# Performance work log

Measured on AMD Instinct MI355X. Metric: run time of the kernel, lower is better.

Reference implementation:

```python
import jax, jax.numpy as jnp
import numpy as np

N_QUBITS = 5
N_A = 1
N_LAYERS = 4
PATCH = 2 ** (N_QUBITS - N_A)  # 16

CNOT4 = jnp.array([[1, 0, 0, 0], [0, 1, 0, 0], [0, 0, 0, 1], [0, 0, 1, 0]], dtype=jnp.complex64)


def _ry(t):
    c = jnp.cos(t / 2).astype(jnp.complex64)
    s = jnp.sin(t / 2).astype(jnp.complex64)
    return jnp.stack([jnp.stack([c, -s]), jnp.stack([s, c])])


def _rot(phi, theta, omega):
    # PennyLane Rot = RZ(omega) RY(theta) RZ(phi)
    c = jnp.cos(theta / 2)
    s = jnp.sin(theta / 2)
    ep = jnp.exp(-0.5j * (phi + omega))  # e^{-i(phi+omega)/2}
    em = jnp.exp(-0.5j * (phi - omega))  # e^{-i(phi-omega)/2}
    return jnp.stack([jnp.stack([ep * c, -jnp.conj(em) * s]),
                      jnp.stack([em * s, jnp.conj(ep) * c])])


def _apply_1q(state, U, w):
    # contract U onto qubit axis w of state [2]*5
    s = jnp.tensordot(U, state, axes=(1, w))
    return jnp.moveaxis(s, 0, w)


def _apply_cnot(state, c, t):
    perm = jnp.moveaxis(state, (c, t), (0, 1))
    shp = perm.shape
    out = (CNOT4 @ perm.reshape(4, -1)).reshape(shp)
    return jnp.moveaxis(out, (0, 1), (c, t))


def _simulate(noise, w):
    # noise: [5], w: [4,5,3] -> normalized probs over first 16 basis states
    state = jnp.zeros((2,) * N_QUBITS, jnp.complex64).at[(0,) * N_QUBITS].set(1.0)
    for q in range(N_QUBITS):
        state = _apply_1q(state, _ry(noise[q]), q)
    for l in range(N_LAYERS):
        r = l % (N_QUBITS - 1) + 1  # StronglyEntanglingLayers default ranges
        for q in range(N_QUBITS):
            state = _apply_1q(state, _rot(w[l, q, 0], w[l, q, 1], w[l, q, 2]), q)
        for q in range(N_QUBITS):
            state = _apply_cnot(state, q, (q + r) % N_QUBITS)
    probs = jnp.abs(state.reshape(-1)) ** 2  # [32]
    p0 = probs[:PATCH] / jnp.sum(probs)  # partial measure: ancilla wire 4 == 0
    return p0 / jnp.max(p0)


def setup_inputs() -> dict:
    key = jax.random.key(0)
    k1, k2 = jax.random.split(key)
    B, G = 65536, 4
    x = jax.random.uniform(k1, (B, N_QUBITS), dtype=jnp.float32)
    weights = jax.random.uniform(k2, (G, N_LAYERS, N_QUBITS, 3), dtype=jnp.float32)  # q_delta=1
    return {"x": x, "weights": weights}


def reference(x, weights):
    sim_g = jax.vmap(_simulate, in_axes=(None, 0))   # over generators
    sim_bg = jax.vmap(sim_g, in_axes=(0, None))      # over batch
    out = sim_bg(x, weights)                         # [B, G, 16]
    return out.reshape(x.shape[0], -1).astype(jnp.float32)  # [B, G*16]
```

## Files before the change

kernel.cpp:

```cpp
#include <hip/hip_runtime.h>


#define NGEN 4
#define NLAY 4
#define NQ   5

typedef _Float16 half8 __attribute__((ext_vector_type(8)));
typedef float    f32x4 __attribute__((ext_vector_type(4)));

__global__ __launch_bounds__(256) void pqg_fused(
    const float* __restrict__ x,
    const float* __restrict__ wts,
    float* __restrict__ out)
{
    __shared__ float gm[NLAY * NQ * 8];
    __shared__ float Mr[16 * 33];
    __shared__ float Mi[16 * 33];
    __shared__ __align__(16) _Float16 afr[512];
    __shared__ __align__(16) _Float16 afi[512];
    __shared__ float scC[512 * 5];
    __shared__ float scS[512 * 5];

    const int t  = threadIdx.x;
    const int g  = blockIdx.x & 3;
    const int b0 = (blockIdx.x >> 2) * 512;

    {
        const float2* xb = (const float2*)(x + (size_t)b0 * 5);
#pragma unroll
        for (int i = 0; i < 5; ++i) {
            const int e = i * 256 + t;
            const float2 v = xb[e];
            scS[2 * e + 0] = __sinf(0.5f * v.x);
            scC[2 * e + 0] = __cosf(0.5f * v.x);
            scS[2 * e + 1] = __sinf(0.5f * v.y);
            scC[2 * e + 1] = __cosf(0.5f * v.y);
        }
    }

    if (t < NLAY * NQ) {
        const float* wp = wts + (g * (NLAY * NQ) + t) * 3;
        const float phi = wp[0], theta = wp[1], omega = wp[2];
        const float a = 0.5f * (phi + omega);
        const float bb = 0.5f * (phi - omega);
        const float h = 0.5f * theta;
        const float sa = __sinf(a), ca = __cosf(a);
        const float sb = __sinf(bb), cb = __cosf(bb);
        const float st = __sinf(h), ct = __cosf(h);
        float* m = &gm[t * 8];
        m[0] =  ca * ct;  m[1] = -sa * ct;
        m[2] = -cb * st;  m[3] = -sb * st;
        m[4] =  cb * st;  m[5] = -sb * st;
        m[6] =  ca * ct;  m[7] =  sa * ct;
    }

#pragma unroll
    for (int h = 0; h < 2; ++h) {
        const int idx = h * 256 + t;
        const int r = idx >> 5, c = idx & 31;
        Mr[r * 33 + c] = (r == c) ? 1.0f : 0.0f;
        Mi[r * 33 + c] = 0.0f;
    }
    __syncthreads();

    const int row = t & 15;
    const int p   = t >> 4;

#pragma clang loop unroll(disable)
    for (int l = NLAY - 1; l >= 0; --l) {
        {
            const int c0 = p, c1 = p + 16;
            int v0 = c0, v1 = c1;
#pragma unroll
            for (int q = 0; q < NQ; ++q) {
                const int cb = 16 >> q;
                int tq = q + l + 1; if (tq >= NQ) tq -= NQ;
                const int tb = 16 >> tq;
                if (v0 & cb) v0 ^= tb;
                if (v1 & cb) v1 ^= tb;
            }
            const float a0r = Mr[row * 33 + v0], a0i = Mi[row * 33 + v0];
            const float a1r = Mr[row * 33 + v1], a1i = Mi[row * 33 + v1];
            __syncthreads();
            Mr[row * 33 + c0] = a0r;  Mi[row * 33 + c0] = a0i;
            Mr[row * 33 + c1] = a1r;  Mi[row * 33 + c1] = a1i;
            __syncthreads();
        }
#pragma clang loop unroll(disable)
        for (int q = NQ - 1; q >= 0; --q) {
            const float* m = &gm[(l * NQ + q) * 8];
            const float u00r = m[0], u00i = m[1], u01r = m[2], u01i = m[3];
            const float u10r = m[4], u10i = m[5], u11r = m[6], u11i = m[7];
            const int sb = 16 >> q;
            const int lowm = sb - 1;
            const int i = ((p & ~lowm) << 1) | (p & lowm);
            const int j = i | sb;
            const int ii = row * 33 + i, jj = row * 33 + j;
            const float ar = Mr[ii], ai = Mi[ii];
            const float br = Mr[jj], bi = Mi[jj];
            Mr[ii] = u00r * ar - u00i * ai + u10r * br - u10i * bi;
            Mi[ii] = u00r * ai + u00i * ar + u10r * bi + u10i * br;
            Mr[jj] = u01r * ar - u01i * ai + u11r * br - u11i * bi;
            Mi[jj] = u01r * ai + u01i * ar + u11r * bi + u11i * br;
            __syncthreads();
        }
    }

#pragma unroll
    for (int h = 0; h < 2; ++h) {
        const int idx = h * 256 + t;
        const int k = idx >> 4, m = idx & 15;
        const int L = (k >> 3) * 16 + m;
        const int jj = k & 7;
        afr[L * 8 + jj] = (_Float16)Mr[m * 33 + k];
        afi[L * 8 + jj] = (_Float16)Mi[m * 33 + k];
    }
    __syncthreads();

    const int lane = t & 63;
    const int wv   = t >> 6;
    const int quad = lane >> 4;
    const int n    = lane & 15;

    const half8 Ar = *(const half8*)&afr[lane * 8];
    const half8 Ai = *(const half8*)&afi[lane * 8];

#pragma unroll
    for (int t8 = 0; t8 < 8; ++t8) {
        const int bl = wv * 128 + t8 * 16 + n;
        const int b  = b0 + bl;
        const float* C = &scC[bl * 5];
        const float* S = &scS[bl * 5];

        const float f01 = ((quad & 2) ? S[0] : C[0]) * ((quad & 1) ? S[1] : C[1]);
        const float a0 = f01 * C[2], a1 = f01 * S[2];
        const float b00 = a0 * C[3], b01 = a0 * S[3];
        const float b10 = a1 * C[3], b11 = a1 * S[3];

        half8 Bf;
        Bf[0] = (_Float16)(b00 * C[4]);  Bf[1] = (_Float16)(b00 * S[4]);
        Bf[2] = (_Float16)(b01 * C[4]);  Bf[3] = (_Float16)(b01 * S[4]);
        Bf[4] = (_Float16)(b10 * C[4]);  Bf[5] = (_Float16)(b10 * S[4]);
        Bf[6] = (_Float16)(b11 * C[4]);  Bf[7] = (_Float16)(b11 * S[4]);

        f32x4 accR = {0.f, 0.f, 0.f, 0.f};
        f32x4 accI = {0.f, 0.f, 0.f, 0.f};
        accR = __builtin_amdgcn_mfma_f32_16x16x32_f16(Ar, Bf, accR, 0, 0, 0);
        accI = __builtin_amdgcn_mfma_f32_16x16x32_f16(Ai, Bf, accI, 0, 0, 0);

        const float p0 = accR[0] * accR[0] + accI[0] * accI[0];
        const float p1 = accR[1] * accR[1] + accI[1] * accI[1];
        const float p2 = accR[2] * accR[2] + accI[2] * accI[2];
        const float p3 = accR[3] * accR[3] + accI[3] * accI[3];

        float mx = fmaxf(fmaxf(p0, p1), fmaxf(p2, p3));
        mx = fmaxf(mx, __shfl_xor(mx, 16));
        mx = fmaxf(mx, __shfl_xor(mx, 32));
        const float inv = 1.0f / mx;

        const float4 o = make_float4(p0 * inv, p1 * inv, p2 * inv, p3 * inv);
        *(float4*)(out + (size_t)b * 64 + g * 16 + quad * 4) = o;
    }
}

extern "C" void kernel_launch(void* const* d_in, const int* in_sizes, int n_in,
                              void* d_out, int out_size, void* d_ws, size_t ws_size,
                              hipStream_t stream) {
    const float* x = (const float*)d_in[0];
    const float* w = (const float*)d_in[1];
    float* out = (float*)d_out;
    const int B = in_sizes[0] / NQ;

    pqg_fused<<<(B / 512) * NGEN, 256, 0, stream>>>(x, w, out);
}
```

Measured before the change: 67.60 us.

## Assign one generator per wavefront and replace block barriers with wave syncs

Each 256-thread block now handles 128 batch rows for all four generators, with each wavefront building one generator's 32x32 circuit matrix independently. Most block-wide __syncthreads calls become wave-level barriers plus an LDS wait. The grid shrinks to B/128 blocks. Per-block matrix construction work per wave rises, with four row updates per lane per gate step, while block barriers go away and the x sin/cos staging is shared across generators. The cost is more shared memory per block and more serial matrix-building work per wave relative to the MFMA phase.

```diff
diff --git a/kernel.cpp b/kernel.cpp
--- a/kernel.cpp
+++ b/kernel.cpp
@@ -8,38 +8,41 @@
 typedef _Float16 half8 __attribute__((ext_vector_type(8)));
 typedef float    f32x4 __attribute__((ext_vector_type(4)));
 
+#define WAVE_SYNC()                                                  \
+    do {                                                             \
+        __builtin_amdgcn_wave_barrier();                             \
+        asm volatile("s_waitcnt lgkmcnt(0)" ::: "memory");           \
+        __builtin_amdgcn_wave_barrier();                             \
+    } while (0)
+
 __global__ __launch_bounds__(256) void pqg_fused(
     const float* __restrict__ x,
     const float* __restrict__ wts,
     float* __restrict__ out)
 {
-    __shared__ float gm[NLAY * NQ * 8];
-    __shared__ float Mr[16 * 33];
-    __shared__ float Mi[16 * 33];
-    __shared__ __align__(16) _Float16 afr[512];
-    __shared__ __align__(16) _Float16 afi[512];
-    __shared__ float scC[512 * 5];
-    __shared__ float scS[512 * 5];
+    __shared__ float gm[NGEN][NLAY * NQ * 8];
+    __shared__ float Mr[NGEN][16 * 33];
+    __shared__ float Mi[NGEN][16 * 33];
+    __shared__ __align__(16) _Float16 afr[NGEN][512];
+    __shared__ __align__(16) _Float16 afi[NGEN][512];
+    __shared__ float scC[640];
+    __shared__ float scS[640];
 
-    const int t  = threadIdx.x;
-    const int g  = blockIdx.x & 3;
-    const int b0 = (blockIdx.x >> 2) * 512;
+    const int t    = threadIdx.x;
+    const int lane = t & 63;
+    const int g    = t >> 6;
+    const int b0   = blockIdx.x * 128;
 
-    {
-        const float2* xb = (const float2*)(x + (size_t)b0 * 5);
-#pragma unroll
-        for (int i = 0; i < 5; ++i) {
-            const int e = i * 256 + t;
-            const float2 v = xb[e];
-            scS[2 * e + 0] = __sinf(0.5f * v.x);
-            scC[2 * e + 0] = __cosf(0.5f * v.x);
-            scS[2 * e + 1] = __sinf(0.5f * v.y);
-            scC[2 * e + 1] = __cosf(0.5f * v.y);
-        }
+    if (t < 160) {
+        const float4 v = ((const float4*)(x + (size_t)b0 * 5))[t];
+        scS[4 * t + 0] = __sinf(0.5f * v.x);  scC[4 * t + 0] = __cosf(0.5f * v.x);
+        scS[4 * t + 1] = __sinf(0.5f * v.y);  scC[4 * t + 1] = __cosf(0.5f * v.y);
+        scS[4 * t + 2] = __sinf(0.5f * v.z);  scC[4 * t + 2] = __cosf(0.5f * v.z);
+        scS[4 * t + 3] = __sinf(0.5f * v.w);  scC[4 * t + 3] = __cosf(0.5f * v.w);
     }
 
-    if (t < NLAY * NQ) {
-        const float* wp = wts + (g * (NLAY * NQ) + t) * 3;
+    if (lane < NLAY * NQ) {
+        const float* wp = wts + (g * (NLAY * NQ) + lane) * 3;
         const float phi = wp[0], theta = wp[1], omega = wp[2];
         const float a = 0.5f * (phi + omega);
         const float bb = 0.5f * (phi - omega);
@@ -47,7 +50,7 @@
         const float sa = __sinf(a), ca = __cosf(a);
         const float sb = __sinf(bb), cb = __cosf(bb);
         const float st = __sinf(h), ct = __cosf(h);
-        float* m = &gm[t * 8];
+        float* m = &gm[g][lane * 8];
         m[0] =  ca * ct;  m[1] = -sa * ct;
         m[2] = -cb * st;  m[3] = -sb * st;
         m[4] =  cb * st;  m[5] = -sb * st;
@@ -55,22 +58,21 @@
     }
 
 #pragma unroll
-    for (int h = 0; h < 2; ++h) {
-        const int idx = h * 256 + t;
+    for (int h = 0; h < 8; ++h) {
+        const int idx = h * 64 + lane;
         const int r = idx >> 5, c = idx & 31;
-        Mr[r * 33 + c] = (r == c) ? 1.0f : 0.0f;
-        Mi[r * 33 + c] = 0.0f;
+        Mr[g][r * 33 + c] = (r == c) ? 1.0f : 0.0f;
+        Mi[g][r * 33 + c] = 0.0f;
     }
-    __syncthreads();
+    WAVE_SYNC();
 
-    const int row = t & 15;
-    const int p   = t >> 4;
+    const int p  = lane & 15;
+    const int rl = lane >> 4;
 
 #pragma clang loop unroll(disable)
     for (int l = NLAY - 1; l >= 0; --l) {
         {
-            const int c0 = p, c1 = p + 16;
-            int v0 = c0, v1 = c1;
+            int v0 = p, v1 = p + 16;
 #pragma unroll
             for (int q = 0; q < NQ; ++q) {
                 const int cb = 16 >> q;
@@ -79,55 +81,71 @@
                 if (v0 & cb) v0 ^= tb;
                 if (v1 & cb) v1 ^= tb;
             }
-            const float a0r = Mr[row * 33 + v0], a0i = Mi[row * 33 + v0];
-            const float a1r = Mr[row * 33 + v1], a1i = Mi[row * 33 + v1];
-            __syncthreads();
-            Mr[row * 33 + c0] = a0r;  Mi[row * 33 + c0] = a0i;
-            Mr[row * 33 + c1] = a1r;  Mi[row * 33 + c1] = a1i;
-            __syncthreads();
+            float tr[8], ti[8];
+#pragma unroll
+            for (int r = 0; r < 4; ++r) {
+                const int row = r * 4 + rl;
+                tr[2 * r + 0] = Mr[g][row * 33 + v0];
+                ti[2 * r + 0] = Mi[g][row * 33 + v0];
+                tr[2 * r + 1] = Mr[g][row * 33 + v1];
+                ti[2 * r + 1] = Mi[g][row * 33 + v1];
+            }
+            WAVE_SYNC();
+#pragma unroll
+            for (int r = 0; r < 4; ++r) {
+                const int row = r * 4 + rl;
+                Mr[g][row * 33 + p]      = tr[2 * r + 0];
+                Mi[g][row * 33 + p]      = ti[2 * r + 0];
+                Mr[g][row * 33 + p + 16] = tr[2 * r + 1];
+                Mi[g][row * 33 + p + 16] = ti[2 * r + 1];
+            }
+            WAVE_SYNC();
         }
 #pragma clang loop unroll(disable)
         for (int q = NQ - 1; q >= 0; --q) {
-            const float* m = &gm[(l * NQ + q) * 8];
+            const float* m = &gm[g][(l * NQ + q) * 8];
             const float u00r = m[0], u00i = m[1], u01r = m[2], u01i = m[3];
             const float u10r = m[4], u10i = m[5], u11r = m[6], u11i = m[7];
             const int sb = 16 >> q;
             const int lowm = sb - 1;
             const int i = ((p & ~lowm) << 1) | (p & lowm);
             const int j = i | sb;
-            const int ii = row * 33 + i, jj = row * 33 + j;
-            const float ar = Mr[ii], ai = Mi[ii];
-            const float br = Mr[jj], bi = Mi[jj];
-            Mr[ii] = u00r * ar - u00i * ai + u10r * br - u10i * bi;
-            Mi[ii] = u00r * ai + u00i * ar + u10r * bi + u10i * br;
-            Mr[jj] = u01r * ar - u01i * ai + u11r * br - u11i * bi;
-            Mi[jj] = u01r * ai + u01i * ar + u11r * bi + u11i * br;
-            __syncthreads();
+#pragma unroll
+            for (int r = 0; r < 4; ++r) {
+                const int row = r * 4 + rl;
+                const int ii = row * 33 + i, jj = row * 33 + j;
+                const float ar = Mr[g][ii], ai = Mi[g][ii];
+                const float br = Mr[g][jj], bi = Mi[g][jj];
+                Mr[g][ii] = u00r * ar - u00i * ai + u10r * br - u10i * bi;
+                Mi[g][ii] = u00r * ai + u00i * ar + u10r * bi + u10i * br;
+                Mr[g][jj] = u01r * ar - u01i * ai + u11r * br - u11i * bi;
+                Mi[g][jj] = u01r * ai + u01i * ar + u11r * bi + u11i * br;
+            }
+            WAVE_SYNC();
         }
     }
 
 #pragma unroll
-    for (int h = 0; h < 2; ++h) {
-        const int idx = h * 256 + t;
+    for (int h = 0; h < 8; ++h) {
+        const int idx = h * 64 + lane;
         const int k = idx >> 4, m = idx & 15;
         const int L = (k >> 3) * 16 + m;
         const int jj = k & 7;
-        afr[L * 8 + jj] = (_Float16)Mr[m * 33 + k];
-        afi[L * 8 + jj] = (_Float16)Mi[m * 33 + k];
+        afr[g][L * 8 + jj] = (_Float16)Mr[g][m * 33 + k];
+        afi[g][L * 8 + jj] = (_Float16)Mi[g][m * 33 + k];
     }
+
     __syncthreads();
 
-    const int lane = t & 63;
-    const int wv   = t >> 6;
     const int quad = lane >> 4;
     const int n    = lane & 15;
 
-    const half8 Ar = *(const half8*)&afr[lane * 8];
-    const half8 Ai = *(const half8*)&afi[lane * 8];
+    const half8 Ar = *(const half8*)&afr[g][lane * 8];
+    const half8 Ai = *(const half8*)&afi[g][lane * 8];
 
 #pragma unroll
     for (int t8 = 0; t8 < 8; ++t8) {
-        const int bl = wv * 128 + t8 * 16 + n;
+        const int bl = t8 * 16 + n;
         const int b  = b0 + bl;
         const float* C = &scC[bl * 5];
         const float* S = &scS[bl * 5];
@@ -171,5 +189,5 @@
     float* out = (float*)d_out;
     const int B = in_sizes[0] / NQ;
 
-    pqg_fused<<<(B / 512) * NGEN, 256, 0, stream>>>(x, w, out);
+    pqg_fused<<<B / 128, 256, 0, stream>>>(x, w, out);
 }
```

After: 75.54 us. 11.7% more time.
